# Optimization experiments

Measured on AMD Instinct MI355X. Metric: run time of the kernel, lower is better.

## Reference

```python
import jax, jax.numpy as jnp
import numpy as np

D = 256          # in_channels == out_channels
H = 4            # num_heads (global branch)
HD = D // H      # head_dim
B = 64           # number of graphs
N = 256          # nodes per graph (max nodes for to_dense_batch)
TOT = B * N      # total nodes
E = TOT * 16     # total edges (avg degree 16)


def _glorot(key, shape):
    fan_in, fan_out = shape[0], shape[1]
    s = jnp.sqrt(6.0 / (fan_in + fan_out))
    return jax.random.uniform(key, shape, jnp.float32, -s, s)


def setup_inputs() -> dict:
    key = jax.random.key(0)
    ks = jax.random.split(key, 20)
    x = jax.random.normal(ks[0], (TOT, D), jnp.float32)
    # intra-graph random edges: local endpoints + graph offset
    local = jax.random.randint(ks[1], (2, E), 0, N)
    gid = jax.random.randint(ks[2], (E,), 0, B)
    edge_index = (local + gid[None, :] * N).astype(jnp.int64)
    batch = (jnp.arange(TOT) // N).astype(jnp.int64)  # sorted, equal-size graphs
    inp = {"x": x, "edge_index": edge_index, "batch": batch}
    # local branch (TransformerConv, heads=1): q/k/v + skip linears [in,out]
    names = ["lq", "lk", "lv", "ls", "gq", "gk", "gv", "go"]
    for i, nm in enumerate(names):
        inp[nm + "_w"] = _glorot(ks[3 + i], (D, D))
        inp[nm + "_b"] = jnp.zeros((D,), jnp.float32)
    inp["w_local"] = jnp.float32(0.5)
    inp["w_global"] = jnp.float32(0.5)
    inp["ln_g"] = jnp.ones((D,), jnp.float32)
    inp["ln_b"] = jnp.zeros((D,), jnp.float32)
    return inp


def _forward(x, edge_index, batch, lq_w, lq_b, lk_w, lk_b, lv_w, lv_b, ls_w, ls_b,
             gq_w, gq_b, gk_w, gk_b, gv_w, gv_b, go_w, go_b,
             w_local, w_global, ln_g, ln_b):
    src, dst = edge_index[0], edge_index[1]
    inv_sqrt_d = 1.0 / jnp.sqrt(jnp.float32(D))

    # ---- local branch: TransformerConv (heads=1, root_weight=True) ----
    q = x @ lq_w + lq_b
    k = x @ lk_w + lk_b
    v = x @ lv_w + lv_b
    logits = jnp.sum(q[dst] * k[src], axis=-1) * inv_sqrt_d          # [E]
    m = jax.ops.segment_max(logits, dst, num_segments=TOT)           # per-target max
    ex = jnp.exp(logits - m[dst])
    den = jax.ops.segment_sum(ex, dst, num_segments=TOT)
    alpha = ex / (den[dst] + 1e-16)
    agg = jax.ops.segment_sum(alpha[:, None] * v[src], dst, num_segments=TOT)
    local_out = agg + x @ ls_w + ls_b                                # skip (root) term

    # ---- global branch: to_dense_batch + masked multihead attention ----
    counts = jax.ops.segment_sum(jnp.ones((TOT,), jnp.float32), batch, num_segments=B)
    starts = (jnp.cumsum(counts) - counts).astype(jnp.int32)
    pos = jnp.arange(TOT, dtype=jnp.int32) - starts[batch]
    dense = jnp.zeros((B, N, D), x.dtype).at[batch, pos].set(x)
    mask = jnp.zeros((B, N), bool).at[batch, pos].set(True)

    qh = (dense @ gq_w + gq_b).reshape(B, N, H, HD)
    kh = (dense @ gk_w + gk_b).reshape(B, N, H, HD)
    vh = (dense @ gv_w + gv_b).reshape(B, N, H, HD)
    scores = jnp.einsum('bnhd,bmhd->bhnm', qh, kh) / jnp.sqrt(jnp.float32(HD))
    scores = jnp.where(mask[:, None, None, :], scores, -jnp.inf)     # mask keys
    attn = jax.nn.softmax(scores, axis=-1)
    od = jnp.einsum('bhnm,bmhd->bnhd', attn, vh).reshape(B, N, D)
    od = od @ go_w + go_b
    global_out = od[batch, pos] + x                                  # in==out residual

    # ---- weighted fusion + residual + LayerNorm ----
    fused = w_local * local_out + w_global * global_out
    out = fused + x
    mu = jnp.mean(out, axis=-1, keepdims=True)
    var = jnp.mean(jnp.square(out - mu), axis=-1, keepdims=True)
    out = (out - mu) / jnp.sqrt(var + 1e-5) * ln_g + ln_b
    return out


def reference(x, edge_index, batch, lq_w, lq_b, lk_w, lk_b, lv_w, lv_b, ls_w, ls_b,
              gq_w, gq_b, gk_w, gk_b, gv_w, gv_b, go_w, go_b,
              w_local, w_global, ln_g, ln_b):
    return _forward(x, edge_index, batch, lq_w, lq_b, lk_w, lk_b, lv_w, lv_b,
                    ls_w, ls_b, gq_w, gq_b, gk_w, gk_b, gv_w, gv_b, go_w, go_b,
                    w_local, w_global, ln_g, ln_b)
```

## Files before the change

kernel.cpp:

```cpp
#include <hip/hip_runtime.h>
#include <hip/hip_bf16.h>

#define D_DIM 256
#define NPG   256
#define HEADS 4
#define HD    64
#define BCAP  64

typedef __bf16 bf16x8 __attribute__((ext_vector_type(8)));
typedef __bf16 bf16x4 __attribute__((ext_vector_type(4)));
typedef float  f32x4  __attribute__((ext_vector_type(4)));

__device__ inline float us2f(unsigned short u) {
    union { unsigned int i; float f; } cv; cv.i = ((unsigned int)u) << 16; return cv.f;
}

#define GLOAD_LDS16(g, l) __builtin_amdgcn_global_load_lds(                    \
    (const __attribute__((address_space(1))) void*)(g),                        \
    (__attribute__((address_space(3))) void*)(l), 16, 0, 0)

__global__ __launch_bounds__(256) void prep_misc(const float* __restrict__ x,
                                                 __bf16* __restrict__ xpk,
        const float* w0, const float* w1, const float* w2, const float* w3,
        const float* w4, const float* w5, const float* w6, const float* w7,
        __bf16* __restrict__ wt, int* __restrict__ zeros, int nb1, int tot) {
    __shared__ __bf16 tile[256][16];
    int bid = blockIdx.x;
    const int t = threadIdx.x;
    if (bid < nb1) {
        const int rt = bid;
        const int ks = t >> 5;
        #pragma unroll
        for (int h2 = 0; h2 < 2; ++h2) {
            int lane = (t & 31) * 2 + h2;
            int row = rt * 16 + (lane & 15);
            int col = ks * 32 + (lane >> 4) * 8;
            const float4* src = reinterpret_cast<const float4*>(x + (size_t)row * 256 + col);
            float4 f0 = src[0], f1 = src[1];
            __bf16* o = xpk + ((size_t)(rt * 8 + ks) * 64 + lane) * 8;
            o[0] = (__bf16)f0.x; o[1] = (__bf16)f0.y; o[2] = (__bf16)f0.z; o[3] = (__bf16)f0.w;
            o[4] = (__bf16)f1.x; o[5] = (__bf16)f1.y; o[6] = (__bf16)f1.z; o[7] = (__bf16)f1.w;
        }
        return;
    }
    bid -= nb1;
    if (bid < 128) {
        const float* Ws[8] = {w0, w1, w2, w3, w4, w5, w6, w7};
        const int jt2 = bid & 15, wsel = bid >> 4;
        const float* W = Ws[wsel];
        const float4* wr = reinterpret_cast<const float4*>(W + (size_t)t * 256 + jt2 * 16);
        #pragma unroll
        for (int u = 0; u < 4; ++u) {
            float4 f = wr[u];
            tile[t][u * 4 + 0] = (__bf16)f.x; tile[t][u * 4 + 1] = (__bf16)f.y;
            tile[t][u * 4 + 2] = (__bf16)f.z; tile[t][u * 4 + 3] = (__bf16)f.w;
        }
        __syncthreads();
        __bf16* out = wt + ((size_t)wsel * 16 + jt2) * 4096;
        #pragma unroll
        for (int u = 0; u < 16; ++u) {
            int e = t * 16 + u;
            int ks = e >> 9, lane = (e >> 3) & 63, i = e & 7;
            int g = lane >> 4, c = lane & 15;
            int k = ks * 32 + g * 8 + i;
            out[e] = tile[k][c];
        }
        return;
    }
    bid -= 128;
    int i = bid * 256 + t;
    if (i < tot) zeros[i] = 0;
}

__global__ __launch_bounds__(512) void proj_csr(const __bf16* __restrict__ xpk,
                                                const __bf16* __restrict__ wt,
        const float* b_gq, const float* b_gk, const float* b_gv,
        const float* b_lq, const float* b_lk, const float* b_lv, const float* b_ls,
        __bf16* o_gq, __bf16* o_gk, __bf16* Vt,
        __bf16* o_lq, __bf16* o_lk, __bf16* o_lv, __bf16* o_ls,
        const int* __restrict__ ei_raw, int* __restrict__ bucket,
        int* __restrict__ deg, int E, int nb_gemm, int M) {
    __shared__ __align__(16) __bf16 wlds[16384];
    int bid = blockIdx.x;
    if (bid >= nb_gemm) {
        int v = ei_raw[2 * (threadIdx.x & 63) + 1];
        unsigned long long nz = __ballot(v != 0);
        bool is64 = (nz == 0ULL);
        int e = (bid - nb_gemm) * 512 + threadIdx.x;
        if (e >= E) return;
        int s, d;
        if (is64) { s = ei_raw[2 * e]; d = ei_raw[2 * (E + e)]; }
        else      { s = ei_raw[e];     d = ei_raw[E + e]; }
        int p = atomicAdd(&deg[d], 1);
        if (p < BCAP) bucket[d * BCAP + p] = s;
        return;
    }
    const int gx = M >> 8;
    const int x = bid % gx;
    const int y = bid / gx;
    const int j = y >> 2;
    const int q = y & 3;
    const int wsel = (j < 3) ? j : j + 1;
    const float* bias = (j == 0) ? b_gq : (j == 1) ? b_gk : (j == 2) ? b_gv :
                        (j == 3) ? b_lq : (j == 4) ? b_lk : (j == 5) ? b_lv : b_ls;
    __bf16* C = (j == 0) ? o_gq : (j == 1) ? o_gk : (j == 2) ? nullptr :
                (j == 3) ? o_lq : (j == 4) ? o_lk : (j == 5) ? o_lv : o_ls;

    {
        const __bf16* gs = wt + (size_t)wsel * 65536 + (size_t)q * 16384;
        #pragma unroll
        for (int it = 0; it < 4; ++it) {
            int chunk = it * 512 + threadIdx.x;
            GLOAD_LDS16(gs + chunk * 8, wlds + chunk * 8);
        }
    }

    const int wid = threadIdx.x >> 6, lane = threadIdx.x & 63;
    const int g = lane >> 4, c = lane & 15;
    const int rt0 = x * 16 + wid * 2;

    const __bf16* ap0 = xpk + ((size_t)rt0 * 8) * 512 + lane * 8;
    const __bf16* ap1 = ap0 + 8 * 512;
    bf16x8 af0 = *reinterpret_cast<const bf16x8*>(ap0);
    bf16x8 af1 = *reinterpret_cast<const bf16x8*>(ap1);

    f32x4 acc[2][4];
    #pragma unroll
    for (int h = 0; h < 2; ++h)
        #pragma unroll
        for (int jt = 0; jt < 4; ++jt) acc[h][jt] = (f32x4){0.f, 0.f, 0.f, 0.f};

    const char* wl = reinterpret_cast<const char*>(wlds) + lane * 16;
    __syncthreads();

    #pragma unroll
    for (int ks = 0; ks < 8; ++ks) {
        bf16x8 nf0, nf1;
        if (ks < 7) {
            nf0 = *reinterpret_cast<const bf16x8*>(ap0 + (ks + 1) * 512);
            nf1 = *reinterpret_cast<const bf16x8*>(ap1 + (ks + 1) * 512);
        }
        #pragma unroll
        for (int jt = 0; jt < 4; ++jt) {
            bf16x8 bf_ = *reinterpret_cast<const bf16x8*>(wl + (jt * 8 + ks) * 1024);
            acc[0][jt] = __builtin_amdgcn_mfma_f32_16x16x32_bf16(bf_, af0, acc[0][jt], 0, 0, 0);
            acc[1][jt] = __builtin_amdgcn_mfma_f32_16x16x32_bf16(bf_, af1, acc[1][jt], 0, 0, 0);
        }
        af0 = nf0; af1 = nf1;
    }
    if (j == 2) {
        #pragma unroll
        for (int h = 0; h < 2; ++h) {
            int m = (rt0 + h) * 16 + c;
            int b = m >> 8, mm = m & 255;
            #pragma unroll
            for (int jt = 0; jt < 4; ++jt) {
                int col0 = q * 64 + jt * 16 + g * 4;
                float4 bv = *reinterpret_cast<const float4*>(bias + col0);
                Vt[(size_t)(b * 256 + col0 + 0) * 256 + mm] = (__bf16)(acc[h][jt][0] + bv.x);
                Vt[(size_t)(b * 256 + col0 + 1) * 256 + mm] = (__bf16)(acc[h][jt][1] + bv.y);
                Vt[(size_t)(b * 256 + col0 + 2) * 256 + mm] = (__bf16)(acc[h][jt][2] + bv.z);
                Vt[(size_t)(b * 256 + col0 + 3) * 256 + mm] = (__bf16)(acc[h][jt][3] + bv.w);
            }
        }
    } else {
        #pragma unroll
        for (int h = 0; h < 2; ++h) {
            int row = (rt0 + h) * 16 + c;
            #pragma unroll
            for (int jt = 0; jt < 4; ++jt) {
                int col0 = q * 64 + jt * 16 + g * 4;
                float4 bv = *reinterpret_cast<const float4*>(bias + col0);
                bf16x4 st;
                st[0] = (__bf16)(acc[h][jt][0] + bv.x);
                st[1] = (__bf16)(acc[h][jt][1] + bv.y);
                st[2] = (__bf16)(acc[h][jt][2] + bv.z);
                st[3] = (__bf16)(acc[h][jt][3] + bv.w);
                *reinterpret_cast<bf16x4*>(&C[(size_t)row * 256 + col0]) = st;
            }
        }
    }
}

__global__ __launch_bounds__(256) void gemm_go(const __bf16* __restrict__ A,
                                               const __bf16* __restrict__ Wp,
                                               const float* __restrict__ bias,
                                               __bf16* __restrict__ C, int M) {
    __shared__ __align__(16) __bf16 wlds[16384];
    {
        const __bf16* gs = Wp + (size_t)blockIdx.y * 16384;
        #pragma unroll
        for (int it = 0; it < 8; ++it) {
            int chunk = it * 256 + threadIdx.x;
            GLOAD_LDS16(gs + chunk * 8, wlds + chunk * 8);
        }
    }
    const int wid = threadIdx.x >> 6, lane = threadIdx.x & 63;
    const int g = lane >> 4, c = lane & 15;
    const int row0 = blockIdx.x * 64 + wid * 16;

    const __bf16* arow = A + (size_t)(row0 + c) * 256 + g * 8;
    bf16x8 af = *reinterpret_cast<const bf16x8*>(arow);

    f32x4 acc[4];
    #pragma unroll
    for (int jt = 0; jt < 4; ++jt) acc[jt] = (f32x4){0.f, 0.f, 0.f, 0.f};

    const char* wl = reinterpret_cast<const char*>(wlds) + lane * 16;
    __syncthreads();
    #pragma unroll
    for (int ks = 0; ks < 8; ++ks) {
        bf16x8 nf;
        if (ks < 7) nf = *reinterpret_cast<const bf16x8*>(arow + (ks + 1) * 32);
        #pragma unroll
        for (int jt = 0; jt < 4; ++jt) {
            bf16x8 bf_ = *reinterpret_cast<const bf16x8*>(wl + (jt * 8 + ks) * 1024);
            acc[jt] = __builtin_amdgcn_mfma_f32_16x16x32_bf16(bf_, af, acc[jt], 0, 0, 0);
        }
        af = nf;
    }
    int row = row0 + c;
    #pragma unroll
    for (int jt = 0; jt < 4; ++jt) {
        int col0 = blockIdx.y * 64 + jt * 16 + g * 4;
        float4 bv = *reinterpret_cast<const float4*>(bias + col0);
        bf16x4 st;
        st[0] = (__bf16)(acc[jt][0] + bv.x);
        st[1] = (__bf16)(acc[jt][1] + bv.y);
        st[2] = (__bf16)(acc[jt][2] + bv.z);
        st[3] = (__bf16)(acc[jt][3] + bv.w);
        *reinterpret_cast<bf16x4*>(&C[(size_t)row * 256 + col0]) = st;
    }
}

__global__ __launch_bounds__(256) void local_attn_bf16(const __bf16* __restrict__ q,
                                                       const __bf16* __restrict__ k,
                                                       const __bf16* __restrict__ v,
                                                       const int* __restrict__ bucket,
                                                       const int* __restrict__ deg,
                                                       __bf16* __restrict__ aggb, int tot) {
    int bid = blockIdx.x;
    bid = (bid & 7) * (gridDim.x >> 3) + (bid >> 3);
    int w = (bid * 256 + (int)threadIdx.x) >> 6;
    int lane = threadIdx.x & 63;
    if (w >= tot) return;
    const int t = w;
    const int g = lane >> 4, cc = lane & 15;

    float qf[16];
    {
        const ushort4* qr = reinterpret_cast<const ushort4*>(q + (size_t)t * 256);
        #pragma unroll
        for (int u = 0; u < 4; ++u) {
            ushort4 qv = qr[cc * 4 + u];
            qf[u * 4 + 0] = us2f(qv.x); qf[u * 4 + 1] = us2f(qv.y);
            qf[u * 4 + 2] = us2f(qv.z); qf[u * 4 + 3] = us2f(qv.w);
        }
    }

    int dg = deg[t];
    if (dg > BCAP) dg = BCAP;
    const int* bkt = bucket + (size_t)t * BCAP;
    float M = -3.0e38f, den = 0.f;
    float a0 = 0.f, a1 = 0.f, a2 = 0.f, a3 = 0.f;

    for (int i0 = 0; i0 < dg; i0 += 4) {
        bool valid = (i0 + g) < dg;
        int s = valid ? bkt[i0 + g] : 0;

        float p = 0.f;
        const ushort4* kr = reinterpret_cast<const ushort4*>(k + (size_t)s * 256);
        #pragma unroll
        for (int u = 0; u < 4; ++u) {
            ushort4 kv = kr[cc * 4 + u];
            p += qf[u * 4 + 0] * us2f(kv.x) + qf[u * 4 + 1] * us2f(kv.y)
               + qf[u * 4 + 2] * us2f(kv.z) + qf[u * 4 + 3] * us2f(kv.w);
        }
        p += __shfl_xor(p, 1); p += __shfl_xor(p, 2);
        p += __shfl_xor(p, 4); p += __shfl_xor(p, 8);

        float lg[4]; int sj[4];
        #pragma unroll
        for (int j = 0; j < 4; ++j) {
            float pj = __shfl(p, j * 16);
            int   ssj = __shfl(s, j * 16);
            bool vj = (i0 + j) < dg;
            lg[j] = vj ? pj * 0.0625f : -3.0e38f;
            sj[j] = vj ? ssj : 0;
        }

        float nM = fmaxf(fmaxf(fmaxf(lg[0], lg[1]), fmaxf(lg[2], lg[3])), M);
        float sc = __expf(M - nM);
        float ex[4];
        #pragma unroll
        for (int j = 0; j < 4; ++j) ex[j] = __expf(lg[j] - nM);

        float s0 = 0.f, s1 = 0.f, s2 = 0.f, s3 = 0.f;
        #pragma unroll
        for (int j = 0; j < 4; ++j) {
            ushort4 vv = reinterpret_cast<const ushort4*>(v + (size_t)sj[j] * 256)[lane];
            s0 += ex[j] * us2f(vv.x); s1 += ex[j] * us2f(vv.y);
            s2 += ex[j] * us2f(vv.z); s3 += ex[j] * us2f(vv.w);
        }
        a0 = a0 * sc + s0; a1 = a1 * sc + s1;
        a2 = a2 * sc + s2; a3 = a3 * sc + s3;
        den = den * sc + ex[0] + ex[1] + ex[2] + ex[3];
        M = nM;
    }
    float inv = (dg > 0) ? 1.0f / den : 0.0f;
    bf16x4 o;
    o[0] = (__bf16)(a0 * inv); o[1] = (__bf16)(a1 * inv);
    o[2] = (__bf16)(a2 * inv); o[3] = (__bf16)(a3 * inv);
    reinterpret_cast<bf16x4*>(aggb + (size_t)t * 256)[lane] = o;
}

__global__ __launch_bounds__(256) void global_attn_mfma(const __bf16* __restrict__ Qb,
                                                        const __bf16* __restrict__ Kb,
                                                        const __bf16* __restrict__ Vt,
                                                        __bf16* __restrict__ od) {
    __shared__ __align__(16) char lds[65536];
    const int tid = threadIdx.x;
    const int wid = tid >> 6, lane = tid & 63;
    const int bh = blockIdx.x >> 2, qq = blockIdx.x & 3;
    const int b = bh >> 2, h = bh & 3;
    const int qb = qq * 4 + wid;
    const int g = lane >> 4, c = lane & 15;

    {
        const __bf16* kgp = Kb + ((size_t)b * 256) * 256 + h * 64;
        int krow = tid >> 3, ch = tid & 7;
        #pragma unroll
        for (int p = 0; p < 8; ++p) {
            int kk = p * 32 + krow;
            bf16x8 val = *reinterpret_cast<const bf16x8*>(kgp + (size_t)kk * 256 + ch * 8);
            int bo = (kk * 128 + ch * 16) ^ ((kk & 7) << 4);
            *reinterpret_cast<bf16x8*>(lds + bo) = val;
        }
    }
    {
        const bf16x8* vgp = reinterpret_cast<const bf16x8*>(Vt + (size_t)bh * 16384);
        #pragma unroll
        for (int p = 0; p < 8; ++p) {
            int off = p * 256 + tid;
            bf16x8 val = vgp[off];
            int row = off >> 5;
            int colb = (off & 31) * 16;
            int bo = 32768 + ((row * 512 + colb) ^ ((row & 7) << 4));
            *reinterpret_cast<bf16x8*>(lds + bo) = val;
        }
    }
    const __bf16* qptr = Qb + ((size_t)(b * 256 + qb * 16 + c)) * 256 + h * 64 + g * 8;
    bf16x8 aq0 = *reinterpret_cast<const bf16x8*>(qptr);
    bf16x8 aq1 = *reinterpret_cast<const bf16x8*>(qptr + 32);
    __syncthreads();

    f32x4 S[16];
    #pragma unroll
    for (int jt = 0; jt < 16; ++jt) S[jt] = (f32x4){0.f, 0.f, 0.f, 0.f};
    #pragma unroll
    for (int jt = 0; jt < 16; ++jt) {
        int key = jt * 16 + c;
        int sw = (key & 7) << 4;
        int bo0 = (key * 128 + g * 16) ^ sw;
        int bo1 = (key * 128 + 64 + g * 16) ^ sw;
        bf16x8 bk0 = *reinterpret_cast<const bf16x8*>(lds + bo0);
        bf16x8 bk1 = *reinterpret_cast<const bf16x8*>(lds + bo1);
        S[jt] = __builtin_amdgcn_mfma_f32_16x16x32_bf16(aq0, bk0, S[jt], 0, 0, 0);
        S[jt] = __builtin_amdgcn_mfma_f32_16x16x32_bf16(aq1, bk1, S[jt], 0, 0, 0);
    }

    float rmax[4] = {-3e38f, -3e38f, -3e38f, -3e38f};
    #pragma unroll
    for (int jt = 0; jt < 16; ++jt)
        #pragma unroll
        for (int r = 0; r < 4; ++r) {
            float s = S[jt][r] * 0.125f;
            S[jt][r] = s;
            rmax[r] = fmaxf(rmax[r], s);
        }
    #pragma unroll
    for (int r = 0; r < 4; ++r) {
        rmax[r] = fmaxf(rmax[r], __shfl_xor(rmax[r], 1));
        rmax[r] = fmaxf(rmax[r], __shfl_xor(rmax[r], 2));
        rmax[r] = fmaxf(rmax[r], __shfl_xor(rmax[r], 4));
        rmax[r] = fmaxf(rmax[r], __shfl_xor(rmax[r], 8));
    }
    float rsum[4] = {0.f, 0.f, 0.f, 0.f};
    #pragma unroll
    for (int jt = 0; jt < 16; ++jt)
        #pragma unroll
        for (int r = 0; r < 4; ++r) {
            float e = __expf(S[jt][r] - rmax[r]);
            S[jt][r] = e;
            rsum[r] += e;
        }
    #pragma unroll
    for (int r = 0; r < 4; ++r) {
        rsum[r] += __shfl_xor(rsum[r], 1);
        rsum[r] += __shfl_xor(rsum[r], 2);
        rsum[r] += __shfl_xor(rsum[r], 4);
        rsum[r] += __shfl_xor(rsum[r], 8);
    }

    __syncthreads();
    char* Pw = lds + wid * 8192;
    #pragma unroll
    for (int jt = 0; jt < 16; ++jt)
        #pragma unroll
        for (int r = 0; r < 4; ++r) {
            int row = g * 4 + r;
            int bo = row * 512 + (jt * 16 + c) * 2;
            bo ^= (row & 7) << 4;
            *reinterpret_cast<__bf16*>(Pw + bo) = (__bf16)S[jt][r];
        }
    __syncthreads();

    f32x4 O[4];
    #pragma unroll
    for (int dt = 0; dt < 4; ++dt) O[dt] = (f32x4){0.f, 0.f, 0.f, 0.f};

    #pragma unroll
    for (int mc = 0; mc < 8; ++mc) {
        int bo = c * 512 + (mc * 32 + g * 8) * 2;
        bo ^= (c & 7) << 4;
        bf16x8 ap = *reinterpret_cast<const bf16x8*>(Pw + bo);
        #pragma unroll
        for (int dt = 0; dt < 4; ++dt) {
            int vrow = dt * 16 + c;
            int vbo = 32768 + ((vrow * 512 + mc * 64 + g * 16) ^ ((vrow & 7) << 4));
            bf16x8 bv = *reinterpret_cast<const bf16x8*>(lds + vbo);
            O[dt] = __builtin_amdgcn_mfma_f32_16x16x32_bf16(ap, bv, O[dt], 0, 0, 0);
        }
    }

    #pragma unroll
    for (int dt = 0; dt < 4; ++dt)
        #pragma unroll
        for (int r = 0; r < 4; ++r) {
            int n = b * 256 + qb * 16 + g * 4 + r;
            int col = h * 64 + dt * 16 + c;
            od[(size_t)n * 256 + col] = (__bf16)(O[dt][r] / rsum[r]);
        }
}

__global__ __launch_bounds__(256) void fuse_ln(const float* __restrict__ x,
                                               const __bf16* __restrict__ aggb,
                                               const __bf16* __restrict__ skipb,
                                               const __bf16* __restrict__ od2b,
                                               const float* __restrict__ wl_p,
                                               const float* __restrict__ wg_p,
                                               const float* __restrict__ gam,
                                               const float* __restrict__ bet,
                                               float* __restrict__ out, int tot) {
    int w = (blockIdx.x * 256 + threadIdx.x) >> 6;
    int lane = threadIdx.x & 63;
    if (w >= tot) return;
    const float wl = wl_p[0], wg = wg_p[0];
    size_t base = (size_t)w * 256;
    float4 xv = reinterpret_cast<const float4*>(x + base)[lane];
    ushort4 ag = reinterpret_cast<const ushort4*>(aggb + base)[lane];
    ushort4 sk = reinterpret_cast<const ushort4*>(skipb + base)[lane];
    ushort4 o2 = reinterpret_cast<const ushort4*>(od2b + base)[lane];
    float v[4];
    v[0] = wl * (us2f(ag.x) + us2f(sk.x)) + wg * (us2f(o2.x) + xv.x) + xv.x;
    v[1] = wl * (us2f(ag.y) + us2f(sk.y)) + wg * (us2f(o2.y) + xv.y) + xv.y;
    v[2] = wl * (us2f(ag.z) + us2f(sk.z)) + wg * (us2f(o2.z) + xv.z) + xv.z;
    v[3] = wl * (us2f(ag.w) + us2f(sk.w)) + wg * (us2f(o2.w) + xv.w) + xv.w;

    float s = v[0] + v[1] + v[2] + v[3];
    #pragma unroll
    for (int off = 32; off; off >>= 1) s += __shfl_xor(s, off);
    float mu = s * (1.0f / 256.0f);
    float e[4], ss = 0.f;
    #pragma unroll
    for (int j = 0; j < 4; ++j) { e[j] = v[j] - mu; ss += e[j] * e[j]; }
    #pragma unroll
    for (int off = 32; off; off >>= 1) ss += __shfl_xor(ss, off);
    float rstd = rsqrtf(ss * (1.0f / 256.0f) + 1e-5f);
    float4 go;
    int c0 = lane * 4;
    go.x = e[0] * rstd * gam[c0 + 0] + bet[c0 + 0];
    go.y = e[1] * rstd * gam[c0 + 1] + bet[c0 + 1];
    go.z = e[2] * rstd * gam[c0 + 2] + bet[c0 + 2];
    go.w = e[3] * rstd * gam[c0 + 3] + bet[c0 + 3];
    reinterpret_cast<float4*>(out + base)[lane] = go;
}

extern "C" void kernel_launch(void* const* d_in, const int* in_sizes, int n_in,
                              void* d_out, int out_size, void* d_ws, size_t ws_size,
                              hipStream_t stream) {
    const float* x    = (const float*)d_in[0];
    const int*   ei   = (const int*)d_in[1];
    const float* lq_w = (const float*)d_in[3];  const float* lq_b = (const float*)d_in[4];
    const float* lk_w = (const float*)d_in[5];  const float* lk_b = (const float*)d_in[6];
    const float* lv_w = (const float*)d_in[7];  const float* lv_b = (const float*)d_in[8];
    const float* ls_w = (const float*)d_in[9];  const float* ls_b = (const float*)d_in[10];
    const float* gq_w = (const float*)d_in[11]; const float* gq_b = (const float*)d_in[12];
    const float* gk_w = (const float*)d_in[13]; const float* gk_b = (const float*)d_in[14];
    const float* gv_w = (const float*)d_in[15]; const float* gv_b = (const float*)d_in[16];
    const float* go_w = (const float*)d_in[17]; const float* go_b = (const float*)d_in[18];
    const float* wl   = (const float*)d_in[19]; const float* wg   = (const float*)d_in[20];
    const float* ln_g = (const float*)d_in[21]; const float* ln_b = (const float*)d_in[22];

    const int TOT = in_sizes[0] / D_DIM;
    const int E = in_sizes[1] / 2;
    const int B = TOT / NPG;
    const size_t S = (size_t)TOT * D_DIM;

    __bf16* xpk   = (__bf16*)d_ws;
    __bf16* qg    = xpk + S;
    __bf16* kg    = qg + S;
    __bf16* aggb  = kg + S;
    __bf16* ql    = aggb + S;
    __bf16* kl    = ql + S;
    __bf16* vl    = kl + S;
    __bf16* skipb = vl + S;
    __bf16* od2b  = skipb + S;
    __bf16* Vt    = od2b + S;
    __bf16* od    = Vt + S;
    __bf16* wt    = od + S;
    int* bucket = (int*)(wt + 8 * 65536);
    int* deg    = bucket + (size_t)TOT * BCAP;

    const int nb1 = TOT / 16;
    const int nbz = (TOT + 255) / 256;
    prep_misc<<<nb1 + 128 + nbz, 256, 0, stream>>>(x, xpk,
        gq_w, gk_w, gv_w, go_w, lq_w, lk_w, lv_w, ls_w, wt, deg, nb1, TOT);

    const int nb_gemm = (TOT / 256) * 28;
    const int nb_edge = (E + 511) / 512;
    proj_csr<<<nb_gemm + nb_edge, 512, 0, stream>>>(xpk, wt,
        gq_b, gk_b, gv_b, lq_b, lk_b, lv_b, ls_b,
        qg, kg, Vt, ql, kl, vl, skipb,
        ei, bucket, deg, E, nb_gemm, TOT);

    global_attn_mfma<<<B * HEADS * 4, 256, 0, stream>>>(qg, kg, Vt, od);

    local_attn_bf16<<<TOT / 4, 256, 0, stream>>>(ql, kl, vl, bucket, deg, aggb, TOT);

    __bf16* wt_go = wt + 3 * 65536;
    gemm_go<<<dim3(TOT / 64, 4), 256, 0, stream>>>(od, wt_go, go_b, od2b, TOT);

    fuse_ln<<<(TOT + 3) / 4, 256, 0, stream>>>(x, aggb, skipb, od2b, wl, wg, ln_g, ln_b,
                                               (float*)d_out, TOT);
}
```

Baseline: 115.9 us.

## Remap proj_csr blocks per XCD and restructure A-fragment prefetch with occupancy hint

Blocks of the projection GEMM are remapped so that consecutive block IDs, which are spread round-robin across the 8 XCDs, land on contiguous row ranges per XCD. The intent is better L2 locality for the shared x tiles. The kernel now loads all eight A fragments for the first row tile up front and processes the two row tiles one after another, reloading fragments for the second tile while the first computes. This lowers accumulator register pressure, and a launch_bounds minimum-blocks hint of 4 is added to raise occupancy. The remap assumes gx is divisible by 8 and risks register spills under the tighter bound.

```diff
diff --git a/kernel.cpp b/kernel.cpp
--- a/kernel.cpp
+++ b/kernel.cpp
@@ -72,8 +72,8 @@
     if (i < tot) zeros[i] = 0;
 }
 
-__global__ __launch_bounds__(512) void proj_csr(const __bf16* __restrict__ xpk,
-                                                const __bf16* __restrict__ wt,
+__global__ __launch_bounds__(512, 4) void proj_csr(const __bf16* __restrict__ xpk,
+                                                   const __bf16* __restrict__ wt,
         const float* b_gq, const float* b_gk, const float* b_gv,
         const float* b_lq, const float* b_lk, const float* b_lv, const float* b_ls,
         __bf16* o_gq, __bf16* o_gk, __bf16* Vt,
@@ -96,8 +96,11 @@
         return;
     }
     const int gx = M >> 8;
-    const int x = bid % gx;
-    const int y = bid / gx;
+    const int chunk = gx >> 3;
+    const int xcd = bid & 7;
+    const int local = bid >> 3;
+    const int x = xcd * chunk + (local % chunk);
+    const int y = local / chunk;
     const int j = y >> 2;
     const int q = y & 3;
     const int wsel = (j < 3) ? j : j + 1;
@@ -110,72 +113,64 @@
         const __bf16* gs = wt + (size_t)wsel * 65536 + (size_t)q * 16384;
         #pragma unroll
         for (int it = 0; it < 4; ++it) {
-            int chunk = it * 512 + threadIdx.x;
-            GLOAD_LDS16(gs + chunk * 8, wlds + chunk * 8);
+            int ch = it * 512 + threadIdx.x;
+            GLOAD_LDS16(gs + ch * 8, wlds + ch * 8);
         }
     }
 
     const int wid = threadIdx.x >> 6, lane = threadIdx.x & 63;
     const int g = lane >> 4, c = lane & 15;
     const int rt0 = x * 16 + wid * 2;
+    const char* wl = reinterpret_cast<const char*>(wlds) + lane * 16;
 
     const __bf16* ap0 = xpk + ((size_t)rt0 * 8) * 512 + lane * 8;
-    const __bf16* ap1 = ap0 + 8 * 512;
-    bf16x8 af0 = *reinterpret_cast<const bf16x8*>(ap0);
-    bf16x8 af1 = *reinterpret_cast<const bf16x8*>(ap1);
-
-    f32x4 acc[2][4];
-    #pragma unroll
-    for (int h = 0; h < 2; ++h)
-        #pragma unroll
-        for (int jt = 0; jt < 4; ++jt) acc[h][jt] = (f32x4){0.f, 0.f, 0.f, 0.f};
-
-    const char* wl = reinterpret_cast<const char*>(wlds) + lane * 16;
+    bf16x8 af[8];
+    #pragma unroll
+    for (int ks = 0; ks < 8; ++ks)
+        af[ks] = *reinterpret_cast<const bf16x8*>(ap0 + ks * 512);
+
     __syncthreads();
 
     #pragma unroll
-    for (int ks = 0; ks < 8; ++ks) {
-        bf16x8 nf0, nf1;
-        if (ks < 7) {
-            nf0 = *reinterpret_cast<const bf16x8*>(ap0 + (ks + 1) * 512);
-            nf1 = *reinterpret_cast<const bf16x8*>(ap1 + (ks + 1) * 512);
-        }
-        #pragma unroll
-        for (int jt = 0; jt < 4; ++jt) {
-            bf16x8 bf_ = *reinterpret_cast<const bf16x8*>(wl + (jt * 8 + ks) * 1024);
-            acc[0][jt] = __builtin_amdgcn_mfma_f32_16x16x32_bf16(bf_, af0, acc[0][jt], 0, 0, 0);
-            acc[1][jt] = __builtin_amdgcn_mfma_f32_16x16x32_bf16(bf_, af1, acc[1][jt], 0, 0, 0);
-        }
-        af0 = nf0; af1 = nf1;
-    }
-    if (j == 2) {
-        #pragma unroll
-        for (int h = 0; h < 2; ++h) {
+    for (int h = 0; h < 2; ++h) {
+        f32x4 acc[4];
+        #pragma unroll
+        for (int jt = 0; jt < 4; ++jt) acc[jt] = (f32x4){0.f, 0.f, 0.f, 0.f};
+        #pragma unroll
+        for (int ks = 0; ks < 8; ++ks) {
+            #pragma unroll
+            for (int jt = 0; jt < 4; ++jt) {
+                bf16x8 bf_ = *reinterpret_cast<const bf16x8*>(wl + (jt * 8 + ks) * 1024);
+                acc[jt] = __builtin_amdgcn_mfma_f32_16x16x32_bf16(bf_, af[ks], acc[jt], 0, 0, 0);
+            }
+            if (h == 0) {
+                const __bf16* ap1 = xpk + ((size_t)(rt0 + 1) * 8) * 512 + lane * 8;
+                af[ks] = *reinterpret_cast<const bf16x8*>(ap1 + ks * 512);
+            }
+        }
+        if (j == 2) {
             int m = (rt0 + h) * 16 + c;
             int b = m >> 8, mm = m & 255;
             #pragma unroll
             for (int jt = 0; jt < 4; ++jt) {
                 int col0 = q * 64 + jt * 16 + g * 4;
                 float4 bv = *reinterpret_cast<const float4*>(bias + col0);
-                Vt[(size_t)(b * 256 + col0 + 0) * 256 + mm] = (__bf16)(acc[h][jt][0] + bv.x);
-                Vt[(size_t)(b * 256 + col0 + 1) * 256 + mm] = (__bf16)(acc[h][jt][1] + bv.y);
-                Vt[(size_t)(b * 256 + col0 + 2) * 256 + mm] = (__bf16)(acc[h][jt][2] + bv.z);
-                Vt[(size_t)(b * 256 + col0 + 3) * 256 + mm] = (__bf16)(acc[h][jt][3] + bv.w);
+                Vt[(size_t)(b * 256 + col0 + 0) * 256 + mm] = (__bf16)(acc[jt][0] + bv.x);
+                Vt[(size_t)(b * 256 + col0 + 1) * 256 + mm] = (__bf16)(acc[jt][1] + bv.y);
+                Vt[(size_t)(b * 256 + col0 + 2) * 256 + mm] = (__bf16)(acc[jt][2] + bv.z);
+                Vt[(size_t)(b * 256 + col0 + 3) * 256 + mm] = (__bf16)(acc[jt][3] + bv.w);
             }
-        }
-    } else {
-        #pragma unroll
-        for (int h = 0; h < 2; ++h) {
+        } else {
             int row = (rt0 + h) * 16 + c;
             #pragma unroll
             for (int jt = 0; jt < 4; ++jt) {
                 int col0 = q * 64 + jt * 16 + g * 4;
                 float4 bv = *reinterpret_cast<const float4*>(bias + col0);
                 bf16x4 st;
-                st[0] = (__bf16)(acc[h][jt][0] + bv.x);
-                st[1] = (__bf16)(acc[h][jt][1] + bv.y);
-                st[2] = (__bf16)(acc[h][jt][2] + bv.z);
-                st[3] = (__bf16)(acc[h][jt][3] + bv.w);
+                st[0] = (__bf16)(acc[jt][0] + bv.x);
+                st[1] = (__bf16)(acc[jt][1] + bv.y);
+                st[2] = (__bf16)(acc[jt][2] + bv.z);
+                st[3] = (__bf16)(acc[jt][3] + bv.w);
                 *reinterpret_cast<bf16x4*>(&C[(size_t)row * 256 + col0]) = st;
             }
         }
```

Measured after the change: 147.0 us. 26.8% more time.
